# Kernel optimization log

Measured on AMD Instinct MI355X. Metric: run time of the kernel, lower is better.

## Reference

```python
import jax, jax.numpy as jnp
import numpy as np

B, CIN, C, H, T = 8, 64, 64, 62, 400
S = 32              # StateSpaceLayer state_dim default
MID = max(1, C // 16)  # ChannelAttention reduction=16


def _dwconv(x, w, pad):
    # x [B,C,H,W], w [C,1,kh,kw], depthwise conv
    return jax.lax.conv_general_dilated(
        x, w, (1, 1), pad,
        dimension_numbers=('NCHW', 'OIHW', 'NCHW'),
        feature_group_count=x.shape[1])


def _pw(x, w):  # 1x1 conv, w [O,C]
    return jnp.einsum('bchw,oc->bohw', x, w)


def _bn(x, g, b):  # eval-mode BatchNorm with running mean=0, var=1 folded into affine
    return x * g[None, :, None, None] + b[None, :, None, None]


def _chan_attn(x, w1, w2):
    # AdaptiveAvg/MaxPool(1) -> shared MLP -> sigmoid gate
    avg = x.mean(axis=(2, 3))
    mx = x.max(axis=(2, 3))
    fc = lambda v: jax.nn.relu(v @ w1.T) @ w2.T  # Linear weights are [out,in]
    a = jax.nn.sigmoid(fc(avg) + fc(mx))
    return x * a[:, :, None, None]


def _spat_attn(x, w):
    avg = x.mean(axis=1, keepdims=True)
    mx = x.max(axis=1, keepdims=True)
    comb = jnp.concatenate([avg, mx], axis=1)  # [B,2,H,W]
    a = jax.nn.sigmoid(jax.lax.conv_general_dilated(
        comb, w, (1, 1), ((3, 3), (3, 3)),
        dimension_numbers=('NCHW', 'OIHW', 'NCHW')))
    return x * a


def _ssm(x, A, Bv, Cm, D, ln_g, ln_b):
    # Faithful to torch: raw reshape [B,C,H,T] -> [B*H, C, T] (row-major, same as torch)
    b, c, h, t = x.shape
    xs = x.reshape(b * h, c, t)
    seq = jnp.moveaxis(xs, 2, 0)  # [T, N, C]

    def step(state, inp):
        state = state @ A.T + Bv               # state = state A^T + B
        out = jax.nn.gelu(state @ Cm + inp * D, approximate=False)
        return state, out

    init = jnp.zeros((b * h, A.shape[0]), x.dtype)
    _, outs = jax.lax.scan(step, init, seq)    # outs [T, N, C]
    out = jnp.moveaxis(outs, 0, 2).reshape(b, c, h, t)
    out = x + out  # residual (dropout p=0)
    # LayerNorm over channel dim
    y = jnp.moveaxis(out, 1, -1)  # [B,H,T,C]
    mu = y.mean(-1, keepdims=True)
    var = ((y - mu) ** 2).mean(-1, keepdims=True)
    y = (y - mu) / jnp.sqrt(var + 1e-5) * ln_g + ln_b
    return jnp.moveaxis(y, -1, 1)


def _half(x, dwdw, dwpw, dwg, dwb, caw1, caw2, saw,
          d1dw, d1pw, d1g, d1b, A, Bv, Cm, D, lng, lnb):
    pad5 = ((2, 2), (2, 2))
    b1 = jax.nn.relu(_bn(_pw(_dwconv(x, dwdw[0], pad5), dwpw[0]), dwg[0], dwb[0]))
    b2 = jax.nn.relu(_bn(_pw(_dwconv(x, dwdw[1], pad5), dwpw[1]), dwg[1], dwb[1]))
    cb = b1 * _chan_attn(b1, caw1, caw2)       # note: x * ChannelAttention(x) as in source
    cb = _bn(_pw(_dwconv(cb, d1dw, ((0, 0), (1, 1))), d1pw), d1g, d1b)
    cb = jax.nn.sigmoid(cb)
    sb = jax.nn.sigmoid(b2 * _spat_attn(b2, saw))
    return _ssm(cb, A, Bv, Cm, D, lng, lnb) * sb


def setup_inputs() -> dict:
    key = jax.random.key(0)
    ks = jax.random.split(key, 16)
    n = lambda k, shp, s=0.1: jax.random.normal(k, shp, dtype=jnp.float32) * s
    return {
        'x': jax.random.normal(ks[0], (B, CIN, H, T), dtype=jnp.float32),
        'in_w': n(ks[1], (C, CIN)),
        'dw2d_dw': n(ks[2], (2, 2, C, 1, 5, 5)),
        'dw2d_pw': n(ks[3], (2, 2, C, C)),
        'dw2d_g': jnp.ones((2, 2, C), jnp.float32),
        'dw2d_b': jnp.zeros((2, 2, C), jnp.float32),
        'ca_w1': n(ks[4], (2, MID, C)),
        'ca_w2': n(ks[5], (2, C, MID)),
        'sa_w': n(ks[6], (2, 1, 2, 7, 7)),
        'dw1d_dw': n(ks[7], (2, C, 1, 1, 3)),
        'dw1d_pw': n(ks[8], (2, C, C)),
        'dw1d_g': jnp.ones((2, C), jnp.float32),
        'dw1d_b': jnp.zeros((2, C), jnp.float32),
        'ssm_A': n(ks[9], (2, S, S)),
        'ssm_B': n(ks[10], (2, S)),
        'ssm_C': n(ks[11], (2, S, C)),
        'ssm_D': n(ks[12], (2, C)),
        'ln_g': jnp.ones((2, C), jnp.float32),
        'ln_b': jnp.zeros((2, C), jnp.float32),
        'out_w': n(ks[13], (C, C)),
        'out_g': jnp.ones((C,), jnp.float32),
        'out_b': jnp.zeros((C,), jnp.float32),
    }


def reference(x, in_w, dw2d_dw, dw2d_pw, dw2d_g, dw2d_b, ca_w1, ca_w2, sa_w,
              dw1d_dw, dw1d_pw, dw1d_g, dw1d_b, ssm_A, ssm_B, ssm_C, ssm_D,
              ln_g, ln_b, out_w, out_g, out_b):
    h = _pw(x, in_w)
    o = _half(h, dw2d_dw[0], dw2d_pw[0], dw2d_g[0], dw2d_b[0], ca_w1[0], ca_w2[0],
              sa_w[0], dw1d_dw[0], dw1d_pw[0], dw1d_g[0], dw1d_b[0],
              ssm_A[0], ssm_B[0], ssm_C[0], ssm_D[0], ln_g[0], ln_b[0])
    o = o[..., ::-1]  # flip time axis
    o = _half(o, dw2d_dw[1], dw2d_pw[1], dw2d_g[1], dw2d_b[1], ca_w1[1], ca_w2[1],
              sa_w[1], dw1d_dw[1], dw1d_pw[1], dw1d_g[1], dw1d_b[1],
              ssm_A[1], ssm_B[1], ssm_C[1], ssm_D[1], ln_g[1], ln_b[1])
    o = o[..., ::-1]
    return jax.nn.relu(_bn(_pw(o, out_w), out_g, out_b))
```

## Files before the change

kernel.cpp:

```cpp
#include <hip/hip_runtime.h>
#include <math.h>

#define DI __device__ __forceinline__

constexpr int B_ = 8, C_ = 64, H_ = 62, T_ = 400, S_ = 32;
constexpr int HT   = H_ * T_;
constexpr int CHT  = C_ * HT;
constexpr int NPOS = B_ * HT;
constexpr int NTOT = B_ * CHT;

typedef __attribute__((ext_vector_type(8))) short short8;
typedef __attribute__((ext_vector_type(4))) float float4v;
typedef unsigned short bh;

DI float sigmoidf_(float x) { return 1.f / (1.f + expf(-x)); }
DI float gelu_(float x) { return 0.5f * x * (1.f + erff(x * 0.70710678118654752f)); }

template<int ACT> DI float act_(float v) {
  if (ACT == 1) return fmaxf(v, 0.f);
  if (ACT == 2) return sigmoidf_(v);
  return v;
}

DI bh f2b(float f) {
  unsigned int u = __float_as_uint(f);
  u += 0x7FFFu + ((u >> 16) & 1u);
  return (bh)(u >> 16);
}
DI float b2f(bh u) { return __uint_as_float(((unsigned int)u) << 16); }
DI unsigned int pk2(float a, float b) {
  return (unsigned int)f2b(a) | ((unsigned int)f2b(b) << 16);
}

__global__ __launch_bounds__(256) void prep(const float* __restrict__ in_w,
    const float* __restrict__ dwpw, const float* __restrict__ dwg,
    const float* __restrict__ d1pw, const float* __restrict__ d1g,
    const float* __restrict__ outw, const float* __restrict__ outg,
    bh* __restrict__ wf) {
  int idx = blockIdx.x * 256 + threadIdx.x;
  int lane = idx & 63, kc = (idx >> 6) & 1, w = (idx >> 7) & 3, slot = idx >> 9;
  const float* src; const float* g;
  switch (slot) {
    case 0: src = in_w;            g = nullptr;      break;
    case 1: src = dwpw + 0 * 4096; g = dwg + 0 * 64; break;
    case 2: src = dwpw + 1 * 4096; g = dwg + 1 * 64; break;
    case 3: src = d1pw + 0 * 4096; g = d1g + 0 * 64; break;
    case 4: src = dwpw + 2 * 4096; g = dwg + 2 * 64; break;
    case 5: src = dwpw + 3 * 4096; g = dwg + 3 * 64; break;
    case 6: src = d1pw + 1 * 4096; g = d1g + 1 * 64; break;
    default: src = outw;           g = outg;         break;
  }
  int o = w * 16 + (lane & 15);
  float gv = g ? g[o] : 1.f;
  unsigned int pack[4];
  #pragma unroll
  for (int h = 0; h < 4; ++h) {
    int c = kc * 32 + (lane >> 4) * 8 + h * 2;
    pack[h] = pk2(src[o * 64 + c] * gv, src[o * 64 + c + 1] * gv);
  }
  *(uint4*)&wf[idx * 8] = make_uint4(pack[0], pack[1], pack[2], pack[3]);
}

template<int ACT, bool REV, bool SPAT, bool DW13, bool INF32, bool OUTF32>
__global__ __launch_bounds__(256) void pwk(const void* __restrict__ in_,
    const bh* __restrict__ wf, const float* __restrict__ bb,
    const float* __restrict__ ac, const float* __restrict__ w3,
    void* __restrict__ out_, float* __restrict__ comb) {
  __shared__ bh Xb[64 * 72];
  const int tid = threadIdx.x;
  const int lane = tid & 63;
  const int wv = tid >> 6;
  const int p0 = blockIdx.x * 64;
  {
    const int ps = (tid & 15) * 4;
    const int cs = (tid >> 4) * 4;
    const int p4 = p0 + ps;
    const int b = p4 / HT, ht = p4 - b * HT;
    const int row = ht / T_, t0 = ht - row * T_;
    unsigned int packed[4][2];
    if constexpr (INF32) {
      const float* rp0 = (const float*)in_ + b * CHT + row * T_;
      float xv[4][4];
      #pragma unroll
      for (int cj = 0; cj < 4; ++cj) {
        const float* rp = rp0 + (cs + cj) * HT;
        if constexpr (REV) {
          float4 u = *(const float4*)&rp[T_ - 4 - t0];
          xv[cj][0] = u.w; xv[cj][1] = u.z; xv[cj][2] = u.y; xv[cj][3] = u.x;
        } else {
          float4 u = *(const float4*)&rp[t0];
          xv[cj][0] = u.x; xv[cj][1] = u.y; xv[cj][2] = u.z; xv[cj][3] = u.w;
        }
      }
      #pragma unroll
      for (int pi = 0; pi < 4; ++pi) {
        packed[pi][0] = pk2(xv[0][pi], xv[1][pi]);
        packed[pi][1] = pk2(xv[2][pi], xv[3][pi]);
      }
    } else if constexpr (DW13) {
      const bh* rp0 = (const bh*)in_ + b * CHT + row * T_;
      float xv[4][4];
      #pragma unroll
      for (int cj = 0; cj < 4; ++cj) {
        const int c = cs + cj;
        const bh* rp = rp0 + c * HT;
        ushort4 u = *(const ushort4*)&rp[t0];
        float x0 = b2f(u.x), x1 = b2f(u.y), x2 = b2f(u.z), x3 = b2f(u.w);
        float xm = (t0 > 0)      ? b2f(rp[t0 - 1]) : 0.f;
        float xp = (t0 < T_ - 4) ? b2f(rp[t0 + 4]) : 0.f;
        float s0 = xm * xm, s1 = x0 * x0, s2 = x1 * x1;
        float s3 = x2 * x2, s4 = x3 * x3, s5 = xp * xp;
        float acv = ac[b * 64 + c];
        float c0 = w3[c * 3 + 0] * acv, c1 = w3[c * 3 + 1] * acv,
              c2 = w3[c * 3 + 2] * acv;
        xv[cj][0] = c0 * s0 + c1 * s1 + c2 * s2;
        xv[cj][1] = c0 * s1 + c1 * s2 + c2 * s3;
        xv[cj][2] = c0 * s2 + c1 * s3 + c2 * s4;
        xv[cj][3] = c0 * s3 + c1 * s4 + c2 * s5;
      }
      #pragma unroll
      for (int pi = 0; pi < 4; ++pi) {
        packed[pi][0] = pk2(xv[0][pi], xv[1][pi]);
        packed[pi][1] = pk2(xv[2][pi], xv[3][pi]);
      }
    } else {
      const bh* rp0 = (const bh*)in_ + b * CHT + row * T_;
      bh us[4][4];
      #pragma unroll
      for (int cj = 0; cj < 4; ++cj) {
        const bh* rp = rp0 + (cs + cj) * HT;
        ushort4 u;
        if constexpr (REV) {
          u = *(const ushort4*)&rp[T_ - 4 - t0];
          us[cj][0] = u.w; us[cj][1] = u.z; us[cj][2] = u.y; us[cj][3] = u.x;
        } else {
          u = *(const ushort4*)&rp[t0];
          us[cj][0] = u.x; us[cj][1] = u.y; us[cj][2] = u.z; us[cj][3] = u.w;
        }
      }
      #pragma unroll
      for (int pi = 0; pi < 4; ++pi) {
        packed[pi][0] = (unsigned int)us[0][pi] | ((unsigned int)us[1][pi] << 16);
        packed[pi][1] = (unsigned int)us[2][pi] | ((unsigned int)us[3][pi] << 16);
      }
    }
    #pragma unroll
    for (int pi = 0; pi < 4; ++pi) {
      int r = ps + pi;
      int col = cs ^ (((r >> 2) & 7) << 3);
      *(uint2*)&Xb[r * 72 + col] = make_uint2(packed[pi][0], packed[pi][1]);
    }
  }
  short8 af0 = *(const short8*)(wf + ((wv * 2 + 0) * 64 + lane) * 8);
  short8 af1 = *(const short8*)(wf + ((wv * 2 + 1) * 64 + lane) * 8);
  const int m4 = (lane >> 4) * 4;
  float binit[4];
  #pragma unroll
  for (int j = 0; j < 4; ++j) binit[j] = bb ? bb[wv * 16 + m4 + j] : 0.f;
  __syncthreads();
  float4v acc[4];
  #pragma unroll
  for (int nt = 0; nt < 4; ++nt) { acc[nt][0] = acc[nt][1] = acc[nt][2] = acc[nt][3] = 0.f; }
  #pragma unroll
  for (int nt = 0; nt < 4; ++nt) {
    int r = nt * 16 + (lane & 15);
    int sw = ((r >> 2) & 7) << 3;
    int cb0 = ((lane >> 4) * 8) ^ sw;
    int cb1 = (32 + (lane >> 4) * 8) ^ sw;
    short8 b0 = *(const short8*)&Xb[r * 72 + cb0];
    short8 b1 = *(const short8*)&Xb[r * 72 + cb1];
    acc[nt] = __builtin_amdgcn_mfma_f32_16x16x32_bf16(af0, b0, acc[nt], 0, 0, 0);
    acc[nt] = __builtin_amdgcn_mfma_f32_16x16x32_bf16(af1, b1, acc[nt], 0, 0, 0);
  }
  float psum[4], pmaxv[4];
  #pragma unroll
  for (int nt = 0; nt < 4; ++nt) {
    int n = nt * 16 + (lane & 15);
    int p = p0 + n;
    int b = p / HT, ht = p - b * HT;
    float s = 0.f, m = -3.4e38f;
    if constexpr (OUTF32) {
      float* op = (float*)out_ + b * CHT + ht + (wv * 16 + m4) * HT;
      #pragma unroll
      for (int j = 0; j < 4; ++j) {
        float r = act_<ACT>(acc[nt][j] + binit[j]);
        op[j * HT] = r;
        if constexpr (SPAT) { s += r; m = fmaxf(m, r); }
      }
    } else {
      bh* op = (bh*)out_ + b * CHT + ht + (wv * 16 + m4) * HT;
      #pragma unroll
      for (int j = 0; j < 4; ++j) {
        float r = act_<ACT>(acc[nt][j] + binit[j]);
        op[j * HT] = f2b(r);
        if constexpr (SPAT) { s += r; m = fmaxf(m, r); }
      }
    }
    if constexpr (SPAT) {
      s += __shfl_xor(s, 16); s += __shfl_xor(s, 32);
      m = fmaxf(m, __shfl_xor(m, 16)); m = fmaxf(m, __shfl_xor(m, 32));
      psum[nt] = s; pmaxv[nt] = m;
    }
  }
  if constexpr (SPAT) {
    __shared__ float redS[4][64], redM[4][64];
    if (lane < 16) {
      #pragma unroll
      for (int nt = 0; nt < 4; ++nt) {
        redS[wv][nt * 16 + lane] = psum[nt];
        redM[wv][nt * 16 + lane] = pmaxv[nt];
      }
    }
    __syncthreads();
    if (tid < 64) {
      float s = redS[0][tid] + redS[1][tid] + redS[2][tid] + redS[3][tid];
      float m = fmaxf(fmaxf(redM[0][tid], redM[1][tid]),
                      fmaxf(redM[2][tid], redM[3][tid]));
      int pp = p0 + tid;
      int b2 = pp / HT, ht2 = pp - b2 * HT;
      comb[b2 * 2 * HT + ht2] = s * (1.f / 64.f);
      comb[b2 * 2 * HT + HT + ht2] = m;
    }
  }
}

__global__ __launch_bounds__(256) void dw5dual(const float* __restrict__ in,
    const float* __restrict__ w0_, const float* __restrict__ w1_,
    bh* __restrict__ out0, bh* __restrict__ out1) {
  const int bc = blockIdx.y;
  const int c = bc & 63;
  int task = blockIdx.x * 256 + threadIdx.x;
  if (task >= 62 * 25) return;
  int h = task / 25;
  int t0 = (task - h * 25) << 4;
  const float* base = in + (size_t)bc * HT;
  const float* wp0 = w0_ + c * 25;
  const float* wp1 = w1_ + c * 25;
  float acc0[16], acc1[16];
  #pragma unroll
  for (int j = 0; j < 16; ++j) { acc0[j] = 0.f; acc1[j] = 0.f; }
  const bool fast = (t0 >= 4) && (t0 <= 380);
  #pragma unroll 1
  for (int u = 0; u < 5; ++u) {
    int hh = h + u - 2;
    if (hh < 0 || hh >= H_) continue;
    const float* row = base + hh * T_;
    float win[24];
    if (fast) {
      #pragma unroll
      for (int j = 0; j < 6; ++j)
        *(float4*)&win[4 * j] = *(const float4*)&row[t0 - 4 + 4 * j];
    } else {
      #pragma unroll
      for (int k = 0; k < 24; ++k) {
        int tt = t0 - 4 + k;
        win[k] = (tt >= 0 && tt < T_) ? row[tt] : 0.f;
      }
    }
    #pragma unroll
    for (int v = 0; v < 5; ++v) {
      float wa = wp0[u * 5 + v];
      float wb = wp1[u * 5 + v];
      #pragma unroll
      for (int j = 0; j < 16; ++j) {
        float x = win[j + v + 2];
        acc0[j] += wa * x;
        acc1[j] += wb * x;
      }
    }
  }
  unsigned int pk0[8], pk1[8];
  #pragma unroll
  for (int j = 0; j < 8; ++j) {
    pk0[j] = pk2(acc0[2 * j], acc0[2 * j + 1]);
    pk1[j] = pk2(acc1[2 * j], acc1[2 * j + 1]);
  }
  bh* o0 = out0 + (size_t)bc * HT + h * T_ + t0;
  bh* o1 = out1 + (size_t)bc * HT + h * T_ + t0;
  *(uint4*)&o0[0] = make_uint4(pk0[0], pk0[1], pk0[2], pk0[3]);
  *(uint4*)&o0[8] = make_uint4(pk0[4], pk0[5], pk0[6], pk0[7]);
  *(uint4*)&o1[0] = make_uint4(pk1[0], pk1[1], pk1[2], pk1[3]);
  *(uint4*)&o1[8] = make_uint4(pk1[4], pk1[5], pk1[6], pk1[7]);
}

__global__ __launch_bounds__(256) void chanred(const bh* __restrict__ in,
    float* __restrict__ sum_, float* __restrict__ max_) {
  int bc = blockIdx.x >> 1, hf = blockIdx.x & 1;
  const bh* base = in + (size_t)bc * HT + hf * (HT / 2);
  float s = 0.f, m = -3.4e38f;
  for (int i = threadIdx.x * 2; i < HT / 2; i += 512) {
    ushort2 q = *(const ushort2*)&base[i];
    float v0 = b2f(q.x), v1 = b2f(q.y);
    s += v0 + v1; m = fmaxf(m, fmaxf(v0, v1));
  }
  #pragma unroll
  for (int off = 32; off > 0; off >>= 1) {
    s += __shfl_down(s, off);
    m = fmaxf(m, __shfl_down(m, off));
  }
  __shared__ float ss[4], sm[4];
  int wv = threadIdx.x >> 6;
  if ((threadIdx.x & 63) == 0) { ss[wv] = s; sm[wv] = m; }
  __syncthreads();
  if (threadIdx.x == 0) {
    float S = ss[0] + ss[1] + ss[2] + ss[3];
    float M = fmaxf(fmaxf(sm[0], sm[1]), fmaxf(sm[2], sm[3]));
    sum_[hf * 512 + bc] = S;
    max_[hf * 512 + bc] = M;
  }
}

__global__ __launch_bounds__(512) void cafc(const float* __restrict__ cs,
    const float* __restrict__ cm, const float* __restrict__ w1,
    const float* __restrict__ w2, float* __restrict__ ac) {
  __shared__ float sa[512], sx[512], hsum[8][4];
  int tid = threadIdx.x;
  sa[tid] = (cs[tid] + cs[512 + tid]) * (1.f / HT);
  sx[tid] = fmaxf(cm[tid], cm[512 + tid]);
  __syncthreads();
  if (tid < 32) {
    int b = tid >> 2, m = tid & 3;
    float s1 = 0.f, s2 = 0.f;
    #pragma unroll
    for (int cc = 0; cc < 64; ++cc) {
      float wv = w1[m * 64 + cc];
      s1 += sa[b * 64 + cc] * wv;
      s2 += sx[b * 64 + cc] * wv;
    }
    hsum[b][m] = fmaxf(s1, 0.f) + fmaxf(s2, 0.f);
  }
  __syncthreads();
  int b = tid >> 6, cc = tid & 63;
  float f = 0.f;
  #pragma unroll
  for (int m = 0; m < 4; ++m) f += hsum[b][m] * w2[cc * 4 + m];
  ac[tid] = sigmoidf_(f);
}

__global__ __launch_bounds__(256) void conv7(const float* __restrict__ comb,
    const float* __restrict__ w, float* __restrict__ as_) {
  __shared__ float sm[2][8][408];
  __shared__ float sw[98];
  const int b = blockIdx.x / 31, hp = blockIdx.x % 31;
  const int h0 = hp * 2;
  const float* cb0 = comb + b * 2 * HT;
  const int tid = threadIdx.x;
  if (tid < 98) sw[tid] = w[tid];
  for (int e = tid; e < 2 * 8 * 408; e += 256) {
    int ci = e / 3264, rem = e - ci * 3264;
    int r = rem / 408, tt = rem - r * 408;
    int hh = h0 - 3 + r, t = tt - 4;
    float v = 0.f;
    if (hh >= 0 && hh < H_ && t >= 0 && t < T_) v = cb0[ci * HT + hh * T_ + t];
    sm[ci][r][tt] = v;
  }
  __syncthreads();
  for (int o = tid; o < 800; o += 256) {
    int oh = o / 400, ot = o - oh * 400;
    float acc = 0.f;
    #pragma unroll
    for (int ci = 0; ci < 2; ++ci)
      #pragma unroll
      for (int u = 0; u < 7; ++u)
        #pragma unroll
        for (int v = 0; v < 7; ++v)
          acc += sw[ci * 49 + u * 7 + v] * sm[ci][oh + u][ot + v + 1];
    as_[b * HT + (h0 + oh) * T_ + ot] = sigmoidf_(acc);
  }
}

__global__ __launch_bounds__(1024) void ssmctA(const float* __restrict__ A_,
    const float* __restrict__ Bv_, float* __restrict__ Pg, float* __restrict__ qg) {
  const int hf = blockIdx.x;
  const float* A = A_ + hf * 1024;
  const float* Bv = Bv_ + hf * 32;
  __shared__ float Pbuf[2][32 * 33];
  __shared__ float qbuf[2][32];
  const int tid = threadIdx.x;
  float* Pc = Pbuf[0]; float* Pn = Pbuf[1];
  float* qc = qbuf[0]; float* qn = qbuf[1];
  Pc[(tid >> 5) * 33 + (tid & 31)] = A[tid];
  if (tid < 32) qc[tid] = Bv[tid];
  __syncthreads();
  for (int i = 0; i < 9; ++i) {
    Pg[(hf * 9 + i) * 1024 + tid] = Pc[(tid >> 5) * 33 + (tid & 31)];
    if (tid < 32) qg[(hf * 9 + i) * 32 + tid] = qc[tid];
    if (i == 8) break;
    const int r = tid >> 5, cc = tid & 31;
    float s0 = 0.f, s1 = 0.f, s2 = 0.f, s3 = 0.f;
    #pragma unroll
    for (int k = 0; k < 32; k += 4) {
      s0 += Pc[r * 33 + k + 0] * Pc[(k + 0) * 33 + cc];
      s1 += Pc[r * 33 + k + 1] * Pc[(k + 1) * 33 + cc];
      s2 += Pc[r * 33 + k + 2] * Pc[(k + 2) * 33 + cc];
      s3 += Pc[r * 33 + k + 3] * Pc[(k + 3) * 33 + cc];
    }
    float qv = 0.f;
    if (tid < 32) {
      float a0 = 0.f, a1 = 0.f;
      #pragma unroll
      for (int k = 0; k < 32; k += 2) {
        a0 += Pc[tid * 33 + k] * qc[k];
        a1 += Pc[tid * 33 + k + 1] * qc[k + 1];
      }
      qv = qc[tid] + a0 + a1;
    }
    Pn[r * 33 + cc] = s0 + s1 + s2 + s3;
    if (tid < 32) qn[tid] = qv;
    __syncthreads();
    float* tp = Pc; Pc = Pn; Pn = tp;
    float* tq = qc; qc = qn; qn = tq;
  }
}

__global__ __launch_bounds__(1024) void ssmctB(const float* __restrict__ Pg,
    const float* __restrict__ qg, const float* __restrict__ Cm_,
    float* __restrict__ ct) {
  const int hf = blockIdx.y;
  __shared__ float P[9][32][33];
  __shared__ float q[9][32];
  __shared__ float Cs[32 * 64];
  __shared__ float st[32][33];
  const int tid = threadIdx.x;
  #pragma unroll
  for (int i = 0; i < 9; ++i) {
    int rem = tid;
    P[i][rem >> 5][rem & 31] = Pg[(hf * 9 + i) * 1024 + rem];
  }
  if (tid < 9 * 32) q[tid >> 5][tid & 31] = qg[hf * 9 * 32 + tid];
  for (int e = tid; e < 2048; e += 1024) Cs[e] = Cm_[hf * 2048 + e];
  __syncthreads();
  const int grp = tid >> 5, j = tid & 31;
  const int tIdx = blockIdx.x * 32 + grp;
  const int n = tIdx + 1;
  float s = 0.f;
  #pragma unroll
  for (int i = 0; i < 9; ++i) {
    st[grp][j] = s;
    float a0 = q[i][j], a1 = 0.f;
    #pragma unroll
    for (int k = 0; k < 32; k += 2) {
      a0 += P[i][j][k] * st[grp][k];
      a1 += P[i][j][k + 1] * st[grp][k + 1];
    }
    s = ((n >> i) & 1) ? (a0 + a1) : s;
  }
  st[grp][j] = s;
  __syncthreads();
  #pragma unroll
  for (int e0 = 0; e0 < 2048; e0 += 1024) {
    int e = e0 + tid;
    int ts = e >> 6, c = e & 63;
    float a0 = 0.f, a1 = 0.f;
    #pragma unroll
    for (int k = 0; k < 32; k += 2) {
      a0 += st[ts][k] * Cs[k * 64 + c];
      a1 += st[ts][k + 1] * Cs[(k + 1) * 64 + c];
    }
    int tg = blockIdx.x * 32 + ts;
    if (tg < T_) ct[(hf * T_ + tg) * 64 + c] = a0 + a1;
  }
}

__global__ __launch_bounds__(256) void k8(const bh* __restrict__ cb,
    const bh* __restrict__ b2, const float* __restrict__ as_,
    const float* __restrict__ ct, const float* __restrict__ D,
    const float* __restrict__ lng, const float* __restrict__ lnb,
    float* __restrict__ out, int rev) {
  __shared__ float ct_s[64 * 65];
  __shared__ float red[4 * 2 * 66];
  const int tid = threadIdx.x;
  const int pl = tid & 63, wg = tid >> 6;
  const int p0 = blockIdx.x * 64;
  #pragma unroll
  for (int k = 0; k < 16; ++k) {
    int idx = k * 256 + tid;
    int r = idx >> 6, c2 = idx & 63;
    int t = (p0 + r) % T_;
    ct_s[r * 65 + c2] = ct[t * C_ + c2];
  }
  const int p = p0 + pl;
  const int b = p / HT, ht = p - b * HT;
  const int h = ht / T_, t = ht - h * T_;
  __syncthreads();
  const bh* cbp = cb + b * CHT + ht;
  const bh* b2p = b2 + b * CHT + ht;
  float o[16];
  float sum = 0.f;
  #pragma unroll
  for (int i = 0; i < 16; ++i) {
    int c = wg * 16 + i;
    float xv = b2f(cbp[c * HT]);
    int c2 = (62 * c + h) & 63;
    float u = ct_s[pl * 65 + c2] + xv * D[c2];
    float v = xv + gelu_(u);
    o[i] = v; sum += v;
  }
  red[wg * 132 + pl] = sum;
  __syncthreads();
  float S = red[0 * 132 + pl] + red[1 * 132 + pl] + red[2 * 132 + pl] + red[3 * 132 + pl];
  float mu = S * (1.f / 64.f);
  float vp = 0.f;
  #pragma unroll
  for (int i = 0; i < 16; ++i) { float d = o[i] - mu; vp += d * d; }
  red[wg * 132 + 66 + pl] = vp;
  __syncthreads();
  float Q = red[0 * 132 + 66 + pl] + red[1 * 132 + 66 + pl] +
            red[2 * 132 + 66 + pl] + red[3 * 132 + 66 + pl];
  float rstd = rsqrtf(Q * (1.f / 64.f) + 1e-5f);
  float av = as_[p];
  int htw = rev ? (h * T_ + (T_ - 1 - t)) : ht;
  float* op = out + b * CHT + htw;
  #pragma unroll
  for (int i = 0; i < 16; ++i) {
    int c = wg * 16 + i;
    float y = (o[i] - mu) * rstd * lng[c] + lnb[c];
    float bv = b2f(b2p[c * HT]);
    op[c * HT] = y * sigmoidf_(bv * bv * av);
  }
}

extern "C" void kernel_launch(void* const* d_in, const int* in_sizes, int n_in,
                              void* d_out, int out_size, void* d_ws, size_t ws_size,
                              hipStream_t stream) {
  const float* x    = (const float*)d_in[0];
  const float* in_w = (const float*)d_in[1];
  const float* dwdw = (const float*)d_in[2];
  const float* dwpw = (const float*)d_in[3];
  const float* dwg  = (const float*)d_in[4];
  const float* dwb  = (const float*)d_in[5];
  const float* caw1 = (const float*)d_in[6];
  const float* caw2 = (const float*)d_in[7];
  const float* saw  = (const float*)d_in[8];
  const float* d1dw = (const float*)d_in[9];
  const float* d1pw = (const float*)d_in[10];
  const float* d1g  = (const float*)d_in[11];
  const float* d1b  = (const float*)d_in[12];
  const float* ssmA = (const float*)d_in[13];
  const float* ssmBv= (const float*)d_in[14];
  const float* ssmC = (const float*)d_in[15];
  const float* ssmD = (const float*)d_in[16];
  const float* lng  = (const float*)d_in[17];
  const float* lnb  = (const float*)d_in[18];
  const float* outw = (const float*)d_in[19];
  const float* outg = (const float*)d_in[20];
  const float* outb = (const float*)d_in[21];

  size_t need = (size_t)3 * NTOT * 4
              + (size_t)(2 * NPOS + NPOS + 1024 + 1024 + 512
                         + 2 * T_ * C_ + 2 * 9 * 1024 + 2 * 9 * 32) * 4
              + (size_t)8 * 4096 * 2;
  if (ws_size < need) return;

  float* W0f = (float*)d_ws;
  bh*    W0b = (bh*)W0f;
  bh*    Fa  = (bh*)(W0f + NTOT);
  bh*    Fb  = (bh*)(W0f + 2 * (size_t)NTOT);
  float* fbase = W0f + 3 * (size_t)NTOT;
  float* comb  = fbase;
  float* as_   = comb + 2 * NPOS;
  float* casum = as_ + NPOS;
  float* camax = casum + 1024;
  float* ac    = camax + 1024;
  float* ct    = ac + 512;
  float* Pg    = ct + 2 * T_ * C_;
  float* qg    = Pg + 2 * 9 * 1024;
  bh* Wbf = (bh*)(qg + 2 * 9 * 32);

  prep<<<16, 256, 0, stream>>>(in_w, dwpw, dwg, d1pw, d1g, outw, outg, Wbf);
  ssmctA<<<2, 1024, 0, stream>>>(ssmA, ssmBv, Pg, qg);
  ssmctB<<<dim3(13, 2), 1024, 0, stream>>>(Pg, qg, ssmC, ct);
  pwk<0, false, false, false, true, true><<<3100, 256, 0, stream>>>(
      x, Wbf + 0 * 4096, nullptr, nullptr, nullptr, W0f, nullptr);

  auto run_half = [&](int hf) {
    const float* dw0 = dwdw + (hf * 2 + 0) * C_ * 25;
    const float* dw1 = dwdw + (hf * 2 + 1) * C_ * 25;
    const float* b0  = dwb + (hf * 2 + 0) * C_;
    const float* b1w = dwb + (hf * 2 + 1) * C_;
    dw5dual<<<dim3(7, 512), 256, 0, stream>>>(W0f, dw0, dw1, Fa, Fb);
    pwk<1, false, false, false, false, false><<<3100, 256, 0, stream>>>(
        Fa, Wbf + (1 + hf * 3) * 4096, b0, nullptr, nullptr, W0b, nullptr);
    pwk<1, false, true, false, false, false><<<3100, 256, 0, stream>>>(
        Fb, Wbf + (2 + hf * 3) * 4096, b1w, nullptr, nullptr, Fa, comb);
    chanred<<<1024, 256, 0, stream>>>(W0b, casum, camax);
    cafc<<<1, 512, 0, stream>>>(casum, camax, caw1 + hf * 4 * 64, caw2 + hf * 64 * 4, ac);
    conv7<<<248, 256, 0, stream>>>(comb, saw + hf * 98, as_);
    pwk<2, false, false, true, false, false><<<3100, 256, 0, stream>>>(
        W0b, Wbf + (3 + hf * 3) * 4096, d1b + hf * C_, ac, d1dw + hf * C_ * 3,
        Fb, nullptr);
    k8<<<3100, 256, 0, stream>>>(Fb, Fa, as_, ct + hf * T_ * C_,
                                 ssmD + hf * C_, lng + hf * C_, lnb + hf * C_,
                                 W0f, hf == 0 ? 1 : 0);
  };

  run_half(0);
  run_half(1);
  pwk<1, true, false, false, true, true><<<3100, 256, 0, stream>>>(
      W0f, Wbf + 7 * 4096, outb, nullptr, nullptr, (float*)d_out, nullptr);
}
```

Baseline: 399.2 us.

## Swap MFMA operands for vectorized stores, bf16 intermediate, double-buffer dwconv rows

The pointwise MFMA kernel now swaps the A/B operand roles so each lane holds four consecutive positions for one output channel. That lets outputs go out as a single float4 or ushort4 store instead of four strided scalar stores, and the spatial sum/max reduction is reworked to use 16-lane shuffles to match. The second half's k8 now writes bf16 instead of fp32, and the final pointwise conv reads that bf16 buffer, which halves that intermediate's traffic at some precision cost. The depthwise 5x5 kernel is unrolled with two row buffers so the next row's loads overlap the current row's FMAs, at the cost of more registers.

Measured after the change: 439.0 us. 10.0% more time.

```diff
diff --git a/kernel.cpp b/kernel.cpp
--- a/kernel.cpp
+++ b/kernel.cpp
@@ -151,64 +151,65 @@
       *(uint2*)&Xb[r * 72 + col] = make_uint2(packed[pi][0], packed[pi][1]);
     }
   }
-  short8 af0 = *(const short8*)(wf + ((wv * 2 + 0) * 64 + lane) * 8);
-  short8 af1 = *(const short8*)(wf + ((wv * 2 + 1) * 64 + lane) * 8);
-  const int m4 = (lane >> 4) * 4;
-  float binit[4];
-  #pragma unroll
-  for (int j = 0; j < 4; ++j) binit[j] = bb ? bb[wv * 16 + m4 + j] : 0.f;
+  short8 bf0 = *(const short8*)(wf + ((wv * 2 + 0) * 64 + lane) * 8);
+  short8 bf1 = *(const short8*)(wf + ((wv * 2 + 1) * 64 + lane) * 8);
+  const int o_l = wv * 16 + (lane & 15);
+  const float bias_l = bb ? bb[o_l] : 0.f;
   __syncthreads();
   float4v acc[4];
   #pragma unroll
-  for (int nt = 0; nt < 4; ++nt) { acc[nt][0] = acc[nt][1] = acc[nt][2] = acc[nt][3] = 0.f; }
-  #pragma unroll
-  for (int nt = 0; nt < 4; ++nt) {
-    int r = nt * 16 + (lane & 15);
+  for (int mt = 0; mt < 4; ++mt) { acc[mt][0] = acc[mt][1] = acc[mt][2] = acc[mt][3] = 0.f; }
+  #pragma unroll
+  for (int mt = 0; mt < 4; ++mt) {
+    int r = mt * 16 + (lane & 15);
     int sw = ((r >> 2) & 7) << 3;
     int cb0 = ((lane >> 4) * 8) ^ sw;
     int cb1 = (32 + (lane >> 4) * 8) ^ sw;
-    short8 b0 = *(const short8*)&Xb[r * 72 + cb0];
-    short8 b1 = *(const short8*)&Xb[r * 72 + cb1];
-    acc[nt] = __builtin_amdgcn_mfma_f32_16x16x32_bf16(af0, b0, acc[nt], 0, 0, 0);
-    acc[nt] = __builtin_amdgcn_mfma_f32_16x16x32_bf16(af1, b1, acc[nt], 0, 0, 0);
-  }
-  float psum[4], pmaxv[4];
-  #pragma unroll
-  for (int nt = 0; nt < 4; ++nt) {
-    int n = nt * 16 + (lane & 15);
-    int p = p0 + n;
-    int b = p / HT, ht = p - b * HT;
-    float s = 0.f, m = -3.4e38f;
+    short8 a0 = *(const short8*)&Xb[r * 72 + cb0];
+    short8 a1 = *(const short8*)&Xb[r * 72 + cb1];
+    acc[mt] = __builtin_amdgcn_mfma_f32_16x16x32_bf16(a0, bf0, acc[mt], 0, 0, 0);
+    acc[mt] = __builtin_amdgcn_mfma_f32_16x16x32_bf16(a1, bf1, acc[mt], 0, 0, 0);
+  }
+  float rs[4][4];
+  #pragma unroll
+  for (int mt = 0; mt < 4; ++mt) {
+    int pp = p0 + mt * 16 + ((lane >> 4) << 2);
+    int b = pp / HT, ht = pp - b * HT;
+    #pragma unroll
+    for (int j = 0; j < 4; ++j) rs[mt][j] = act_<ACT>(acc[mt][j] + bias_l);
     if constexpr (OUTF32) {
-      float* op = (float*)out_ + b * CHT + ht + (wv * 16 + m4) * HT;
-      #pragma unroll
-      for (int j = 0; j < 4; ++j) {
-        float r = act_<ACT>(acc[nt][j] + binit[j]);
-        op[j * HT] = r;
-        if constexpr (SPAT) { s += r; m = fmaxf(m, r); }
-      }
+      float* op = (float*)out_ + b * CHT + (size_t)o_l * HT + ht;
+      *(float4*)op = make_float4(rs[mt][0], rs[mt][1], rs[mt][2], rs[mt][3]);
     } else {
-      bh* op = (bh*)out_ + b * CHT + ht + (wv * 16 + m4) * HT;
-      #pragma unroll
-      for (int j = 0; j < 4; ++j) {
-        float r = act_<ACT>(acc[nt][j] + binit[j]);
-        op[j * HT] = f2b(r);
-        if constexpr (SPAT) { s += r; m = fmaxf(m, r); }
-      }
-    }
-    if constexpr (SPAT) {
-      s += __shfl_xor(s, 16); s += __shfl_xor(s, 32);
-      m = fmaxf(m, __shfl_xor(m, 16)); m = fmaxf(m, __shfl_xor(m, 32));
-      psum[nt] = s; pmaxv[nt] = m;
+      bh* op = (bh*)out_ + b * CHT + (size_t)o_l * HT + ht;
+      ushort4 r4;
+      r4.x = f2b(rs[mt][0]); r4.y = f2b(rs[mt][1]);
+      r4.z = f2b(rs[mt][2]); r4.w = f2b(rs[mt][3]);
+      *(ushort4*)op = r4;
     }
   }
   if constexpr (SPAT) {
     __shared__ float redS[4][64], redM[4][64];
-    if (lane < 16) {
-      #pragma unroll
-      for (int nt = 0; nt < 4; ++nt) {
-        redS[wv][nt * 16 + lane] = psum[nt];
-        redM[wv][nt * 16 + lane] = pmaxv[nt];
+    #pragma unroll
+    for (int mt = 0; mt < 4; ++mt) {
+      float s[4], m[4];
+      #pragma unroll
+      for (int j = 0; j < 4; ++j) { s[j] = rs[mt][j]; m[j] = rs[mt][j]; }
+      #pragma unroll
+      for (int mask = 1; mask < 16; mask <<= 1) {
+        #pragma unroll
+        for (int j = 0; j < 4; ++j) {
+          s[j] += __shfl_xor(s[j], mask);
+          m[j] = fmaxf(m[j], __shfl_xor(m[j], mask));
+        }
+      }
+      if ((lane & 15) == 0) {
+        int pl = mt * 16 + ((lane >> 4) << 2);
+        #pragma unroll
+        for (int j = 0; j < 4; ++j) {
+          redS[wv][pl + j] = s[j];
+          redM[wv][pl + j] = m[j];
+        }
       }
     }
     __syncthreads();
@@ -240,35 +241,46 @@
   #pragma unroll
   for (int j = 0; j < 16; ++j) { acc0[j] = 0.f; acc1[j] = 0.f; }
   const bool fast = (t0 >= 4) && (t0 <= 380);
-  #pragma unroll 1
-  for (int u = 0; u < 5; ++u) {
-    int hh = h + u - 2;
-    if (hh < 0 || hh >= H_) continue;
-    const float* row = base + hh * T_;
-    float win[24];
-    if (fast) {
-      #pragma unroll
-      for (int j = 0; j < 6; ++j)
-        *(float4*)&win[4 * j] = *(const float4*)&row[t0 - 4 + 4 * j];
+  auto loadrow = [&](int hh, float* wb) {
+    if (hh >= 0 && hh < H_) {
+      const float* row = base + hh * T_;
+      if (fast) {
+        #pragma unroll
+        for (int j = 0; j < 6; ++j)
+          *(float4*)&wb[4 * j] = *(const float4*)&row[t0 - 4 + 4 * j];
+      } else {
+        #pragma unroll
+        for (int k = 0; k < 24; ++k) {
+          int tt = t0 - 4 + k;
+          wb[k] = (tt >= 0 && tt < T_) ? row[tt] : 0.f;
+        }
+      }
     } else {
       #pragma unroll
-      for (int k = 0; k < 24; ++k) {
-        int tt = t0 - 4 + k;
-        win[k] = (tt >= 0 && tt < T_) ? row[tt] : 0.f;
-      }
-    }
+      for (int k = 0; k < 24; ++k) wb[k] = 0.f;
+    }
+  };
+  auto dorow = [&](int u, const float* wb) {
     #pragma unroll
     for (int v = 0; v < 5; ++v) {
       float wa = wp0[u * 5 + v];
-      float wb = wp1[u * 5 + v];
+      float wx = wp1[u * 5 + v];
       #pragma unroll
       for (int j = 0; j < 16; ++j) {
-        float x = win[j + v + 2];
+        float x = wb[j + v + 2];
         acc0[j] += wa * x;
-        acc1[j] += wb * x;
-      }
-    }
-  }
+        acc1[j] += wx * x;
+      }
+    }
+  };
+  float wA[24], wB[24];
+  loadrow(h - 2, wA);
+  loadrow(h - 1, wB);
+  dorow(0, wA); loadrow(h + 0, wA);
+  dorow(1, wB); loadrow(h + 1, wB);
+  dorow(2, wA); loadrow(h + 2, wA);
+  dorow(3, wB);
+  dorow(4, wA);
   unsigned int pk0[8], pk1[8];
   #pragma unroll
   for (int j = 0; j < 8; ++j) {
@@ -462,11 +474,12 @@
   }
 }
 
+template<bool OUTF32>
 __global__ __launch_bounds__(256) void k8(const bh* __restrict__ cb,
     const bh* __restrict__ b2, const float* __restrict__ as_,
     const float* __restrict__ ct, const float* __restrict__ D,
     const float* __restrict__ lng, const float* __restrict__ lnb,
-    float* __restrict__ out, int rev) {
+    void* __restrict__ out, int rev) {
   __shared__ float ct_s[64 * 65];
   __shared__ float red[4 * 2 * 66];
   const int tid = threadIdx.x;
@@ -510,13 +523,14 @@
   float rstd = rsqrtf(Q * (1.f / 64.f) + 1e-5f);
   float av = as_[p];
   int htw = rev ? (h * T_ + (T_ - 1 - t)) : ht;
-  float* op = out + b * CHT + htw;
   #pragma unroll
   for (int i = 0; i < 16; ++i) {
     int c = wg * 16 + i;
     float y = (o[i] - mu) * rstd * lng[c] + lnb[c];
     float bv = b2f(b2p[c * HT]);
-    op[c * HT] = y * sigmoidf_(bv * bv * av);
+    float r = y * sigmoidf_(bv * bv * av);
+    if constexpr (OUTF32) ((float*)out)[b * CHT + htw + c * HT] = r;
+    else                  ((bh*)out)[b * CHT + htw + c * HT] = f2b(r);
   }
 }
 
@@ -589,13 +603,18 @@
     pwk<2, false, false, true, false, false><<<3100, 256, 0, stream>>>(
         W0b, Wbf + (3 + hf * 3) * 4096, d1b + hf * C_, ac, d1dw + hf * C_ * 3,
         Fb, nullptr);
-    k8<<<3100, 256, 0, stream>>>(Fb, Fa, as_, ct + hf * T_ * C_,
-                                 ssmD + hf * C_, lng + hf * C_, lnb + hf * C_,
-                                 W0f, hf == 0 ? 1 : 0);
+    if (hf == 0)
+      k8<true><<<3100, 256, 0, stream>>>(Fb, Fa, as_, ct + hf * T_ * C_,
+                                         ssmD + hf * C_, lng + hf * C_,
+                                         lnb + hf * C_, W0f, 1);
+    else
+      k8<false><<<3100, 256, 0, stream>>>(Fb, Fa, as_, ct + hf * T_ * C_,
+                                          ssmD + hf * C_, lng + hf * C_,
+                                          lnb + hf * C_, W0b, 0);
   };
 
   run_half(0);
   run_half(1);
-  pwk<1, true, false, false, true, true><<<3100, 256, 0, stream>>>(
-      W0f, Wbf + 7 * 4096, outb, nullptr, nullptr, (float*)d_out, nullptr);
-}
+  pwk<1, true, false, false, false, true><<<3100, 256, 0, stream>>>(
+      W0b, Wbf + 7 * 4096, outb, nullptr, nullptr, (float*)d_out, nullptr);
+}
```

## Double pointwise-conv tile to 128 positions and store final half output as bf16

Applied to the files above, without the earlier changes.

The pointwise MFMA kernel now processes 128 positions per block instead of 64. Each thread loads 8 channels and writes 16-byte LDS stores, and the grid is halved. Separately, the second-half k8 kernel writes bf16 instead of fp32, and the final output projection reads that bf16 buffer, cutting memory traffic on both sides. The trade-offs are more registers and accumulators per thread, which may lower occupancy, plus one extra bf16 rounding before the final projection.

New measurement: 399.6 us. Within noise of the previous version (+0.1%).

```diff
diff --git a/kernel.cpp b/kernel.cpp
--- a/kernel.cpp
+++ b/kernel.cpp
@@ -66,23 +66,22 @@
     const bh* __restrict__ wf, const float* __restrict__ bb,
     const float* __restrict__ ac, const float* __restrict__ w3,
     void* __restrict__ out_, float* __restrict__ comb) {
-  __shared__ bh Xb[64 * 72];
+  __shared__ bh Xb[128 * 72];
   const int tid = threadIdx.x;
   const int lane = tid & 63;
   const int wv = tid >> 6;
-  const int p0 = blockIdx.x * 64;
+  const int p0 = blockIdx.x * 128;
   {
-    const int ps = (tid & 15) * 4;
-    const int cs = (tid >> 4) * 4;
+    const int ps = (tid & 31) * 4;
+    const int cs = (tid >> 5) * 8;
     const int p4 = p0 + ps;
     const int b = p4 / HT, ht = p4 - b * HT;
     const int row = ht / T_, t0 = ht - row * T_;
-    unsigned int packed[4][2];
+    float xv[8][4];
     if constexpr (INF32) {
       const float* rp0 = (const float*)in_ + b * CHT + row * T_;
-      float xv[4][4];
-      #pragma unroll
-      for (int cj = 0; cj < 4; ++cj) {
+      #pragma unroll
+      for (int cj = 0; cj < 8; ++cj) {
         const float* rp = rp0 + (cs + cj) * HT;
         if constexpr (REV) {
           float4 u = *(const float4*)&rp[T_ - 4 - t0];
@@ -92,16 +91,10 @@
           xv[cj][0] = u.x; xv[cj][1] = u.y; xv[cj][2] = u.z; xv[cj][3] = u.w;
         }
       }
-      #pragma unroll
-      for (int pi = 0; pi < 4; ++pi) {
-        packed[pi][0] = pk2(xv[0][pi], xv[1][pi]);
-        packed[pi][1] = pk2(xv[2][pi], xv[3][pi]);
-      }
     } else if constexpr (DW13) {
       const bh* rp0 = (const bh*)in_ + b * CHT + row * T_;
-      float xv[4][4];
-      #pragma unroll
-      for (int cj = 0; cj < 4; ++cj) {
+      #pragma unroll
+      for (int cj = 0; cj < 8; ++cj) {
         const int c = cs + cj;
         const bh* rp = rp0 + c * HT;
         ushort4 u = *(const ushort4*)&rp[t0];
@@ -118,37 +111,33 @@
         xv[cj][2] = c0 * s2 + c1 * s3 + c2 * s4;
         xv[cj][3] = c0 * s3 + c1 * s4 + c2 * s5;
       }
-      #pragma unroll
-      for (int pi = 0; pi < 4; ++pi) {
-        packed[pi][0] = pk2(xv[0][pi], xv[1][pi]);
-        packed[pi][1] = pk2(xv[2][pi], xv[3][pi]);
-      }
     } else {
       const bh* rp0 = (const bh*)in_ + b * CHT + row * T_;
-      bh us[4][4];
-      #pragma unroll
-      for (int cj = 0; cj < 4; ++cj) {
+      #pragma unroll
+      for (int cj = 0; cj < 8; ++cj) {
         const bh* rp = rp0 + (cs + cj) * HT;
         ushort4 u;
         if constexpr (REV) {
           u = *(const ushort4*)&rp[T_ - 4 - t0];
-          us[cj][0] = u.w; us[cj][1] = u.z; us[cj][2] = u.y; us[cj][3] = u.x;
+          xv[cj][0] = b2f(u.w); xv[cj][1] = b2f(u.z);
+          xv[cj][2] = b2f(u.y); xv[cj][3] = b2f(u.x);
         } else {
           u = *(const ushort4*)&rp[t0];
-          us[cj][0] = u.x; us[cj][1] = u.y; us[cj][2] = u.z; us[cj][3] = u.w;
+          xv[cj][0] = b2f(u.x); xv[cj][1] = b2f(u.y);
+          xv[cj][2] = b2f(u.z); xv[cj][3] = b2f(u.w);
         }
-      }
-      #pragma unroll
-      for (int pi = 0; pi < 4; ++pi) {
-        packed[pi][0] = (unsigned int)us[0][pi] | ((unsigned int)us[1][pi] << 16);
-        packed[pi][1] = (unsigned int)us[2][pi] | ((unsigned int)us[3][pi] << 16);
       }
     }
     #pragma unroll
     for (int pi = 0; pi < 4; ++pi) {
       int r = ps + pi;
       int col = cs ^ (((r >> 2) & 7) << 3);
-      *(uint2*)&Xb[r * 72 + col] = make_uint2(packed[pi][0], packed[pi][1]);
+      uint4 w4;
+      w4.x = pk2(xv[0][pi], xv[1][pi]);
+      w4.y = pk2(xv[2][pi], xv[3][pi]);
+      w4.z = pk2(xv[4][pi], xv[5][pi]);
+      w4.w = pk2(xv[6][pi], xv[7][pi]);
+      *(uint4*)&Xb[r * 72 + col] = w4;
     }
   }
   short8 af0 = *(const short8*)(wf + ((wv * 2 + 0) * 64 + lane) * 8);
@@ -158,11 +147,11 @@
   #pragma unroll
   for (int j = 0; j < 4; ++j) binit[j] = bb ? bb[wv * 16 + m4 + j] : 0.f;
   __syncthreads();
-  float4v acc[4];
-  #pragma unroll
-  for (int nt = 0; nt < 4; ++nt) { acc[nt][0] = acc[nt][1] = acc[nt][2] = acc[nt][3] = 0.f; }
-  #pragma unroll
-  for (int nt = 0; nt < 4; ++nt) {
+  float4v acc[8];
+  #pragma unroll
+  for (int nt = 0; nt < 8; ++nt) { acc[nt][0] = acc[nt][1] = acc[nt][2] = acc[nt][3] = 0.f; }
+  #pragma unroll
+  for (int nt = 0; nt < 8; ++nt) {
     int r = nt * 16 + (lane & 15);
     int sw = ((r >> 2) & 7) << 3;
     int cb0 = ((lane >> 4) * 8) ^ sw;
@@ -172,9 +161,9 @@
     acc[nt] = __builtin_amdgcn_mfma_f32_16x16x32_bf16(af0, b0, acc[nt], 0, 0, 0);
     acc[nt] = __builtin_amdgcn_mfma_f32_16x16x32_bf16(af1, b1, acc[nt], 0, 0, 0);
   }
-  float psum[4], pmaxv[4];
-  #pragma unroll
-  for (int nt = 0; nt < 4; ++nt) {
+  float psum[8], pmaxv[8];
+  #pragma unroll
+  for (int nt = 0; nt < 8; ++nt) {
     int n = nt * 16 + (lane & 15);
     int p = p0 + n;
     int b = p / HT, ht = p - b * HT;
@@ -203,16 +192,16 @@
     }
   }
   if constexpr (SPAT) {
-    __shared__ float redS[4][64], redM[4][64];
+    __shared__ float redS[4][128], redM[4][128];
     if (lane < 16) {
       #pragma unroll
-      for (int nt = 0; nt < 4; ++nt) {
+      for (int nt = 0; nt < 8; ++nt) {
         redS[wv][nt * 16 + lane] = psum[nt];
         redM[wv][nt * 16 + lane] = pmaxv[nt];
       }
     }
     __syncthreads();
-    if (tid < 64) {
+    if (tid < 128) {
       float s = redS[0][tid] + redS[1][tid] + redS[2][tid] + redS[3][tid];
       float m = fmaxf(fmaxf(redM[0][tid], redM[1][tid]),
                       fmaxf(redM[2][tid], redM[3][tid]));
@@ -462,11 +451,12 @@
   }
 }
 
+template<bool OUTF32>
 __global__ __launch_bounds__(256) void k8(const bh* __restrict__ cb,
     const bh* __restrict__ b2, const float* __restrict__ as_,
     const float* __restrict__ ct, const float* __restrict__ D,
     const float* __restrict__ lng, const float* __restrict__ lnb,
-    float* __restrict__ out, int rev) {
+    void* __restrict__ out, int rev) {
   __shared__ float ct_s[64 * 65];
   __shared__ float red[4 * 2 * 66];
   const int tid = threadIdx.x;
@@ -510,13 +500,14 @@
   float rstd = rsqrtf(Q * (1.f / 64.f) + 1e-5f);
   float av = as_[p];
   int htw = rev ? (h * T_ + (T_ - 1 - t)) : ht;
-  float* op = out + b * CHT + htw;
   #pragma unroll
   for (int i = 0; i < 16; ++i) {
     int c = wg * 16 + i;
     float y = (o[i] - mu) * rstd * lng[c] + lnb[c];
     float bv = b2f(b2p[c * HT]);
-    op[c * HT] = y * sigmoidf_(bv * bv * av);
+    float r = y * sigmoidf_(bv * bv * av);
+    if constexpr (OUTF32) ((float*)out)[b * CHT + htw + c * HT] = r;
+    else                  ((bh*)out)[b * CHT + htw + c * HT] = f2b(r);
   }
 }
 
@@ -570,7 +561,7 @@
   prep<<<16, 256, 0, stream>>>(in_w, dwpw, dwg, d1pw, d1g, outw, outg, Wbf);
   ssmctA<<<2, 1024, 0, stream>>>(ssmA, ssmBv, Pg, qg);
   ssmctB<<<dim3(13, 2), 1024, 0, stream>>>(Pg, qg, ssmC, ct);
-  pwk<0, false, false, false, true, true><<<3100, 256, 0, stream>>>(
+  pwk<0, false, false, false, true, true><<<1550, 256, 0, stream>>>(
       x, Wbf + 0 * 4096, nullptr, nullptr, nullptr, W0f, nullptr);
 
   auto run_half = [&](int hf) {
@@ -579,23 +570,28 @@
     const float* b0  = dwb + (hf * 2 + 0) * C_;
     const float* b1w = dwb + (hf * 2 + 1) * C_;
     dw5dual<<<dim3(7, 512), 256, 0, stream>>>(W0f, dw0, dw1, Fa, Fb);
-    pwk<1, false, false, false, false, false><<<3100, 256, 0, stream>>>(
+    pwk<1, false, false, false, false, false><<<1550, 256, 0, stream>>>(
         Fa, Wbf + (1 + hf * 3) * 4096, b0, nullptr, nullptr, W0b, nullptr);
-    pwk<1, false, true, false, false, false><<<3100, 256, 0, stream>>>(
+    pwk<1, false, true, false, false, false><<<1550, 256, 0, stream>>>(
         Fb, Wbf + (2 + hf * 3) * 4096, b1w, nullptr, nullptr, Fa, comb);
     chanred<<<1024, 256, 0, stream>>>(W0b, casum, camax);
     cafc<<<1, 512, 0, stream>>>(casum, camax, caw1 + hf * 4 * 64, caw2 + hf * 64 * 4, ac);
     conv7<<<248, 256, 0, stream>>>(comb, saw + hf * 98, as_);
-    pwk<2, false, false, true, false, false><<<3100, 256, 0, stream>>>(
+    pwk<2, false, false, true, false, false><<<1550, 256, 0, stream>>>(
         W0b, Wbf + (3 + hf * 3) * 4096, d1b + hf * C_, ac, d1dw + hf * C_ * 3,
         Fb, nullptr);
-    k8<<<3100, 256, 0, stream>>>(Fb, Fa, as_, ct + hf * T_ * C_,
-                                 ssmD + hf * C_, lng + hf * C_, lnb + hf * C_,
-                                 W0f, hf == 0 ? 1 : 0);
+    if (hf == 0)
+      k8<true><<<3100, 256, 0, stream>>>(Fb, Fa, as_, ct + hf * T_ * C_,
+                                         ssmD + hf * C_, lng + hf * C_,
+                                         lnb + hf * C_, W0f, 1);
+    else
+      k8<false><<<3100, 256, 0, stream>>>(Fb, Fa, as_, ct + hf * T_ * C_,
+                                          ssmD + hf * C_, lng + hf * C_,
+                                          lnb + hf * C_, W0b, 0);
   };
 
   run_half(0);
   run_half(1);
-  pwk<1, true, false, false, true, true><<<3100, 256, 0, stream>>>(
-      W0f, Wbf + 7 * 4096, outb, nullptr, nullptr, (float*)d_out, nullptr);
-}
+  pwk<1, true, false, false, false, true><<<1550, 256, 0, stream>>>(
+      W0b, Wbf + 7 * 4096, outb, nullptr, nullptr, (float*)d_out, nullptr);
+}
```
